# Kernel tuning notes

Hardware: AMD Instinct MI355X
Metric: run time of the kernel (lower is better)

Reference implementation:

```python
import jax, jax.numpy as jnp
import numpy as np

DEPTH = 4      # truncation depth of the signature
DIM = 8        # path channels
PATH_LEN = 16384
STREAM = True


def _restricted_exp(z, depth):
    # exp(z) in truncated tensor algebra: level k term = z^{\otimes k}/k!, flattened to [d**k]
    terms = [z]
    for k in range(2, depth + 1):
        terms.append((terms[-1][:, None] * z[None, :]).reshape(-1) / k)
    return tuple(terms)


def _chen_mult(a, b, depth):
    # Truncated tensor-algebra product (Chen's relation); a_0 = b_0 = 1 implicit.
    # c_k = a_k + b_k + sum_{i=1}^{k-1} a_i \otimes b_{k-i}
    c = []
    for k in range(depth):
        t = a[k] + b[k]
        for i in range(k):
            t = t + (a[i][:, None] * b[k - 1 - i][None, :]).reshape(-1)
        c.append(t)
    return tuple(c)


def setup_inputs() -> dict:
    key = jax.random.key(0)
    path = jax.random.normal(key, (PATH_LEN, DIM), dtype=jnp.float32)
    return {"path": path}


def reference(path):
    depth = DEPTH
    d = path.shape[-1]
    inc = path[1:] - path[:-1]                                # [N-1, d] increments
    exps = jax.vmap(lambda z: _restricted_exp(z, depth))(inc)  # tuple of [N-1, d**k]
    init = tuple(jnp.zeros((d ** (k + 1),), dtype=path.dtype) for k in range(depth))

    def step(carry, x):
        new = _chen_mult(carry, x, depth)
        return new, (new if STREAM else None)

    last, ys = jax.lax.scan(step, init, exps)
    if STREAM:
        # flatten: concat levels -> [N-1, d + d^2 + ... + d^depth]
        return jnp.concatenate([y for y in ys], axis=-1)
    return jnp.concatenate(last, axis=-1)
```

## Files before the change

### kernel.cpp

```cpp
#include <hip/hip_runtime.h>

#define NPATH 16384
#define DIM   8
#define NINC  (NPATH - 1)
#define SIG   4680
#define L1OFF 0
#define L2OFF 8
#define L3OFF 72
#define L4OFF 584
#define NCHUNK 256
#define CHUNK  64
#define NSUB  1024
#define SUB   16
#define SPC   4
#define NGRP  16
#define GSIZE 16
#define C6    0.16666666666666666f
#define LPAD  17

typedef float vfloat4 __attribute__((ext_vector_type(4)));
typedef float vfloat2 __attribute__((ext_vector_type(2)));


__device__ __forceinline__ void light_barrier() {
  asm volatile("s_waitcnt lgkmcnt(0)" ::: "memory");
  __builtin_amdgcn_s_barrier();
}

__device__ __forceinline__ void zero_state(float r4[16], float r3[2],
                                           float& a1i, float& a2v,
                                           float& a2s, float& a1s, float& a1t) {
#pragma unroll
  for (int l = 0; l < 16; ++l) r4[l] = 0.f;
  r3[0] = r3[1] = 0.f;
  a1i = a2v = a2s = a1s = a1t = 0.f;
}

__device__ __forceinline__ void store_sig_reg(float* __restrict__ dst,
                                              const float r4[16], const float r3[2],
                                              float a2s, float a1t, int t) {
  float4* d4 = (float4*)(dst + L4OFF + 16 * t);
  d4[0] = make_float4(r4[0], r4[1], r4[2], r4[3]);
  d4[1] = make_float4(r4[4], r4[5], r4[6], r4[7]);
  d4[2] = make_float4(r4[8], r4[9], r4[10], r4[11]);
  d4[3] = make_float4(r4[12], r4[13], r4[14], r4[15]);
  *(float2*)(dst + L3OFF + 2 * t) = make_float2(r3[0], r3[1]);
  if (t < 64) dst[L2OFF + t] = a2s;
  if (t < 8)  dst[L1OFF + t] = a1t;
}

struct ChenB {
  float4 B0, B1, B2, B3;
  float4 C0, C1, C2, C3;
  float4 D0, D1, D2, D3;
  float4 E0, E1;
  float2 b3c, b2jk, b1k;
  float  b2ij, b1j, b1i, b2t, b1j2, b1i2, b1t;
};

__device__ __forceinline__ void chen_load(const float* __restrict__ b, int t, ChenB& R) {
  const int i   = t >> 5;
  const int j   = (t >> 2) & 7;
  const int ij  = t >> 2;
  const int c0  = 2 * t;
  const int jk0 = c0 & 63;
  const int k0  = 2 * (t & 3);
  const int i2  = t >> 3;
  const int j2  = t & 7;
  const float4* bv = (const float4*)b;
  R.B0 = bv[146 + 4 * t]; R.B1 = bv[147 + 4 * t]; R.B2 = bv[148 + 4 * t]; R.B3 = bv[149 + 4 * t];
  R.C0 = bv[18 + 2 * jk0]; R.C1 = bv[19 + 2 * jk0]; R.C2 = bv[20 + 2 * jk0]; R.C3 = bv[21 + 2 * jk0];
  R.D0 = bv[2 + 2 * k0]; R.D1 = bv[3 + 2 * k0]; R.D2 = bv[4 + 2 * k0]; R.D3 = bv[5 + 2 * k0];
  R.E0 = bv[0]; R.E1 = bv[1];
  R.b3c  = *(const float2*)(b + L3OFF + c0);
  R.b2jk = *(const float2*)(b + L2OFF + jk0);
  R.b1k  = *(const float2*)(b + L1OFF + k0);
  R.b2ij = b[L2OFF + ij];
  R.b1j  = b[L1OFF + j];
  R.b1i  = b[L1OFF + i];
  R.b2t = 0.f; R.b1j2 = 0.f; R.b1i2 = 0.f; R.b1t = 0.f;
  if (t < 64) { R.b2t = b[L2OFF + t]; R.b1j2 = b[L1OFF + j2]; R.b1i2 = b[L1OFF + i2]; }
  if (t < 8)  { R.b1t = b[L1OFF + t]; }
}

__device__ __forceinline__ void chen_apply(float r4[16], float r3[2],
                                           float& a1i, float& a2v,
                                           float& a2s, float& a1s, float& a1t,
                                           const ChenB& R, int t) {
  const float b4r[16] = {R.B0.x,R.B0.y,R.B0.z,R.B0.w, R.B1.x,R.B1.y,R.B1.z,R.B1.w,
                         R.B2.x,R.B2.y,R.B2.z,R.B2.w, R.B3.x,R.B3.y,R.B3.z,R.B3.w};
  const float b3r[16] = {R.C0.x,R.C0.y,R.C0.z,R.C0.w, R.C1.x,R.C1.y,R.C1.z,R.C1.w,
                         R.C2.x,R.C2.y,R.C2.z,R.C2.w, R.C3.x,R.C3.y,R.C3.z,R.C3.w};
  const float b2r[16] = {R.D0.x,R.D0.y,R.D0.z,R.D0.w, R.D1.x,R.D1.y,R.D1.z,R.D1.w,
                         R.D2.x,R.D2.y,R.D2.z,R.D2.w, R.D3.x,R.D3.y,R.D3.z,R.D3.w};
  const float b1r[8]  = {R.E0.x,R.E0.y,R.E0.z,R.E0.w, R.E1.x,R.E1.y,R.E1.z,R.E1.w};
#pragma unroll
  for (int l = 0; l < 8; ++l) {
    r4[l]     += b4r[l]     + a1i * b3r[l]     + a2v * b2r[l]     + r3[0] * b1r[l];
    r4[8 + l] += b4r[8 + l] + a1i * b3r[8 + l] + a2v * b2r[8 + l] + r3[1] * b1r[l];
  }
  r3[0] += R.b3c.x + a1i * R.b2jk.x + a2v * R.b1k.x;
  r3[1] += R.b3c.y + a1i * R.b2jk.y + a2v * R.b1k.y;
  const float a1i_old = a1i;
  a2v += R.b2ij + a1i_old * R.b1j;
  if (t < 64) { a2s += R.b2t + a1s * R.b1j2; a1s += R.b1i2; }
  a1i = a1i_old + R.b1i;
  if (t < 8) a1t += R.b1t;
}

__device__ __forceinline__ void step_update(const float* zs,
                                            float r4[16], float r3[2],
                                            float& a1i, float& a2v,
                                            float& a2s, float& a1s, float& a1t, int t) {
  const int i  = t >> 5;
  const int j  = (t >> 2) & 7;
  const int k0 = 2 * (t & 3);
  const int i2 = t >> 3;
  const int j2 = t & 7;
  const float zi = zs[i];
  const float zj = zs[j];
  const float2 zk = *(const float2*)(zs + k0);
  const float4 za = *(const float4*)zs;
  const float4 zb = *(const float4*)(zs + 4);
  const float zn[8] = {za.x, za.y, za.z, za.w, zb.x, zb.y, zb.z, zb.w};
  const float a1zi4 = a1i + 0.25f * zi;
  const float zj6   = C6 * zj;
  const float T0 = r3[0] + a2v * (0.5f * zk.x) + a1zi4 * (zj6 * zk.x);
  const float T1 = r3[1] + a2v * (0.5f * zk.y) + a1zi4 * (zj6 * zk.y);
  const float U  = a2v + (0.5f * a1i + C6 * zi) * zj;
#pragma unroll
  for (int l = 0; l < 8; ++l) {
    r4[l]     += T0 * zn[l];
    r4[8 + l] += T1 * zn[l];
  }
  r3[0] += zk.x * U;
  r3[1] += zk.y * U;
  a2v += (a1i + 0.5f * zi) * zj;
  a1i += zi;
  if (t < 64) {
    const float zi2 = zs[i2], zj2v = zs[j2];
    a2s += (a1s + 0.5f * zi2) * zj2v;
    a1s += zi2;
  }
  if (t < 8) a1t += zs[t];
}

__global__ __launch_bounds__(256) void k_totals(const float* __restrict__ path,
                                                float* __restrict__ T64,
                                                float* __restrict__ snap) {
  __shared__ float zbuf[CHUNK][8];
  const int t = threadIdx.x;
  const int b = blockIdx.x;
  const int base = b * CHUNK;
  for (int u = t; u < CHUNK * 8; u += 256) {
    const int s = u >> 3, l = u & 7;
    const int rB = min(base + s + 1, NPATH - 1);
    zbuf[s][l] = path[rB * DIM + l] - path[(base + s) * DIM + l];
  }
  float r4[16], r3[2], a1i, a2v, a2s, a1s, a1t;
  zero_state(r4, r3, a1i, a2v, a2s, a1s, a1t);
  __syncthreads();
  for (int w = 0; w < SPC; ++w) {
    if (w > 0) store_sig_reg(snap + ((size_t)b * SPC + w) * SIG, r4, r3, a2s, a1t, t);
#pragma unroll
    for (int s2 = 0; s2 < SUB; ++s2)
      step_update(zbuf[SUB * w + s2], r4, r3, a1i, a2v, a2s, a1s, a1t, t);
  }
  store_sig_reg(T64 + (size_t)b * SIG, r4, r3, a2s, a1t, t);
}

__global__ __launch_bounds__(256) void k_scan(const float* __restrict__ in,
                                              float* __restrict__ prefout,
                                              float* __restrict__ totout,
                                              int count) {
  const int t = threadIdx.x;
  const size_t goff = (size_t)blockIdx.x * count;
  float r4[16], r3[2], a1i, a2v, a2s, a1s, a1t;
  zero_state(r4, r3, a1i, a2v, a2s, a1s, a1t);
  ChenB bA, bB;
  chen_load(in + goff * SIG, t, bA);
  for (int m = 0; m < count; m += 2) {
    if (m + 1 < count) chen_load(in + (goff + m + 1) * SIG, t, bB);
    store_sig_reg(prefout + (goff + m) * SIG, r4, r3, a2s, a1t, t);
    chen_apply(r4, r3, a1i, a2v, a2s, a1s, a1t, bA, t);
    if (m + 1 >= count) break;
    if (m + 2 < count) chen_load(in + (goff + m + 2) * SIG, t, bA);
    store_sig_reg(prefout + (goff + m + 1) * SIG, r4, r3, a2s, a1t, t);
    chen_apply(r4, r3, a1i, a2v, a2s, a1s, a1t, bB, t);
  }
  if (totout != nullptr) store_sig_reg(totout + (size_t)blockIdx.x * SIG, r4, r3, a2s, a1t, t);
}

__global__ __launch_bounds__(256) void k_out(const float* __restrict__ path,
                                             const float* __restrict__ pref,
                                             const float* __restrict__ GT,
                                             const float* __restrict__ snap,
                                             float* __restrict__ out) {
  __shared__ float zbuf[SUB][8];
  __shared__ __align__(16) float lbuf[2][256 * LPAD];
  const int t = threadIdx.x;
  const int sIdx = blockIdx.x;
  const int b = sIdx >> 2;
  const int g = b >> 4;
  const int base = sIdx * SUB;
  const int n = min(SUB, NINC - base);
  if (t < SUB * 8) {
    const int s = t >> 3, l = t & 7;
    const int rB = min(base + s + 1, NPATH - 1);
    zbuf[s][l] = path[rB * DIM + l] - path[(base + s) * DIM + l];
  }
  float r4[16], r3[2], a1i, a2v, a2s, a1s, a1t;
  zero_state(r4, r3, a1i, a2v, a2s, a1s, a1t);
  const int cnt = g + 1 + ((sIdx & 3) ? 1 : 0);
#define PADDR(m) ((m) < g ? GT + (size_t)(m) * SIG \
                          : ((m) == g ? pref + (size_t)b * SIG : snap + (size_t)sIdx * SIG))
  ChenB cA, cB;
  chen_load(PADDR(0), t, cA);
  for (int m = 0; m < cnt; m += 2) {
    if (m + 1 < cnt) chen_load(PADDR(m + 1), t, cB);
    chen_apply(r4, r3, a1i, a2v, a2s, a1s, a1t, cA, t);
    if (m + 1 >= cnt) break;
    if (m + 2 < cnt) chen_load(PADDR(m + 2), t, cA);
    chen_apply(r4, r3, a1i, a2v, a2s, a1s, a1t, cB, t);
  }
#undef PADDR
  __syncthreads();
  const int tp = t >> 2;
  const int rq = 4 * (t & 3);
#pragma unroll 4
  for (int s2 = 0; s2 < n; ++s2) {
    step_update(zbuf[s2], r4, r3, a1i, a2v, a2s, a1s, a1t, t);
    float* lb = lbuf[s2 & 1] + LPAD * t;
    *(float4*)(lb + 0)  = make_float4(r4[0], r4[1], r4[2], r4[3]);
    *(float4*)(lb + 4)  = make_float4(r4[4], r4[5], r4[6], r4[7]);
    *(float4*)(lb + 8)  = make_float4(r4[8], r4[9], r4[10], r4[11]);
    *(float4*)(lb + 12) = make_float4(r4[12], r4[13], r4[14], r4[15]);
    light_barrier();
    const float* lbr = lbuf[s2 & 1];
    float* dst = out + (size_t)(base + s2) * SIG;
#pragma unroll
    for (int q = 0; q < 4; ++q) {
      const vfloat4 v = *(const vfloat4*)(lbr + LPAD * (tp + 64 * q) + rq);
      __builtin_nontemporal_store(v, (vfloat4*)(dst + L4OFF + 4 * t + 1024 * q));
    }
    vfloat2 r3v; r3v.x = r3[0]; r3v.y = r3[1];
    __builtin_nontemporal_store(r3v, (vfloat2*)(dst + L3OFF + 2 * t));
    if (t < 64) __builtin_nontemporal_store(a2s, dst + L2OFF + t);
    if (t < 8)  __builtin_nontemporal_store(a1t, dst + L1OFF + t);
  }
}

extern "C" void kernel_launch(void* const* d_in, const int* in_sizes, int n_in,
                              void* d_out, int out_size, void* d_ws, size_t ws_size,
                              hipStream_t stream) {
  (void)in_sizes; (void)n_in; (void)out_size; (void)ws_size;
  const float* path = (const float*)d_in[0];
  float* out = (float*)d_out;
  float* ws = (float*)d_ws;

  float* T64    = ws;
  float* pref   = T64    + (size_t)NCHUNK * SIG;
  float* GT     = pref   + (size_t)NCHUNK * SIG;
  float* snap   = GT     + (size_t)NGRP * SIG;

  k_totals<<<NCHUNK, 256, 0, stream>>>(path, T64, snap);
  k_scan<<<NGRP, 256, 0, stream>>>(T64, pref, GT, GSIZE);
  k_out<<<NSUB, 256, 0, stream>>>(path, pref, GT, snap, out);
}
```

Before: 134.4 us.

## Remap k_out thread ownership so level-4 stores are direct without LDS transpose

Changes how level-3/4 signature elements are assigned to threads in the output kernel so each thread owns the contiguous float4 chunks it writes. The per-step LDS staging buffer and block barrier are removed, and a new Chen load/apply variant is written for the new mapping. Each thread now keeps redundant copies of lower-level state (four a1/a2/r3 values), which costs some extra registers and arithmetic per step.

```diff
diff --git a/kernel.cpp b/kernel.cpp
--- a/kernel.cpp
+++ b/kernel.cpp
@@ -16,16 +16,9 @@
 #define NGRP  16
 #define GSIZE 16
 #define C6    0.16666666666666666f
-#define LPAD  17
 
 typedef float vfloat4 __attribute__((ext_vector_type(4)));
-typedef float vfloat2 __attribute__((ext_vector_type(2)));
-
-
-__device__ __forceinline__ void light_barrier() {
-  asm volatile("s_waitcnt lgkmcnt(0)" ::: "memory");
-  __builtin_amdgcn_s_barrier();
-}
+
 
 __device__ __forceinline__ void zero_state(float r4[16], float r3[2],
                                            float& a1i, float& a2v,
@@ -191,13 +184,70 @@
   if (totout != nullptr) store_sig_reg(totout + (size_t)blockIdx.x * SIG, r4, r3, a2s, a1t, t);
 }
 
+
+struct ChenBN {
+  float4 B[4];
+  float4 C3r, D2r, E1r;
+  float  b3c[4];
+  float  b2jk, b1k, b1j;
+  float  b2ij[4];
+  float  b1i[4];
+  float  b2t, b1j2, b1i2, b1t;
+};
+
+__device__ __forceinline__ void chen_loadN(const float* __restrict__ b, int t, ChenBN& R) {
+  const int h  = t & 1;
+  const int th = t >> 1;
+  const int kk = th & 7;
+  const int jj = (th >> 3) & 7;
+  const int i0 = th >> 6;
+  const int jk = th & 63;
+#pragma unroll
+  for (int q = 0; q < 4; ++q) {
+    const int cq = th + 128 * q;
+    R.B[q]    = *(const float4*)(b + L4OFF + 8 * cq + 4 * h);
+    R.b3c[q]  = b[L3OFF + cq];
+    R.b2ij[q] = b[L2OFF + (i0 + 2 * q) * 8 + jj];
+    R.b1i[q]  = b[L1OFF + i0 + 2 * q];
+  }
+  R.C3r = *(const float4*)(b + L3OFF + 8 * jk + 4 * h);
+  R.D2r = *(const float4*)(b + L2OFF + 8 * kk + 4 * h);
+  R.E1r = *(const float4*)(b + L1OFF + 4 * h);
+  R.b2jk = b[L2OFF + jk];
+  R.b1k  = b[L1OFF + kk];
+  R.b1j  = b[L1OFF + jj];
+  R.b2t = 0.f; R.b1j2 = 0.f; R.b1i2 = 0.f; R.b1t = 0.f;
+  if (t < 64) { R.b2t = b[L2OFF + t]; R.b1j2 = b[L1OFF + (t & 7)]; R.b1i2 = b[L1OFF + (t >> 3)]; }
+  if (t < 8)  { R.b1t = b[L1OFF + t]; }
+}
+
+__device__ __forceinline__ void chen_applyN(float r4n[16], float r3n[4],
+                                            float a1n[4], float a2n[4],
+                                            float& a2s, float& a1s, float& a1t,
+                                            const ChenBN& R, int t) {
+  const float c3[4] = {R.C3r.x, R.C3r.y, R.C3r.z, R.C3r.w};
+  const float d2[4] = {R.D2r.x, R.D2r.y, R.D2r.z, R.D2r.w};
+  const float e1[4] = {R.E1r.x, R.E1r.y, R.E1r.z, R.E1r.w};
+#pragma unroll
+  for (int q = 0; q < 4; ++q) {
+    const float b4q[4] = {R.B[q].x, R.B[q].y, R.B[q].z, R.B[q].w};
+#pragma unroll
+    for (int u = 0; u < 4; ++u)
+      r4n[4 * q + u] += b4q[u] + a1n[q] * c3[u] + a2n[q] * d2[u] + r3n[q] * e1[u];
+    r3n[q] += R.b3c[q] + a1n[q] * R.b2jk + a2n[q] * R.b1k;
+    a2n[q] += R.b2ij[q] + a1n[q] * R.b1j;
+    a1n[q] += R.b1i[q];
+  }
+  if (t < 64) { a2s += R.b2t + a1s * R.b1j2; a1s += R.b1i2; }
+  if (t < 8)  a1t += R.b1t;
+}
+
 __global__ __launch_bounds__(256) void k_out(const float* __restrict__ path,
                                              const float* __restrict__ pref,
                                              const float* __restrict__ GT,
                                              const float* __restrict__ snap,
                                              float* __restrict__ out) {
   __shared__ float zbuf[SUB][8];
-  __shared__ __align__(16) float lbuf[2][256 * LPAD];
   const int t = threadIdx.x;
   const int sIdx = blockIdx.x;
   const int b = sIdx >> 2;
@@ -209,42 +259,67 @@
     const int rB = min(base + s + 1, NPATH - 1);
     zbuf[s][l] = path[rB * DIM + l] - path[(base + s) * DIM + l];
   }
-  float r4[16], r3[2], a1i, a2v, a2s, a1s, a1t;
-  zero_state(r4, r3, a1i, a2v, a2s, a1s, a1t);
+  const int h  = t & 1;
+  const int th = t >> 1;
+  const int kk = th & 7;
+  const int jj = (th >> 3) & 7;
+  const int i0 = th >> 6;
+  float r4n[16], r3n[4], a1n[4], a2n[4];
+#pragma unroll
+  for (int l = 0; l < 16; ++l) r4n[l] = 0.f;
+#pragma unroll
+  for (int q = 0; q < 4; ++q) { r3n[q] = 0.f; a1n[q] = 0.f; a2n[q] = 0.f; }
+  float a2s = 0.f, a1s = 0.f, a1t = 0.f;
   const int cnt = g + 1 + ((sIdx & 3) ? 1 : 0);
 #define PADDR(m) ((m) < g ? GT + (size_t)(m) * SIG \
                           : ((m) == g ? pref + (size_t)b * SIG : snap + (size_t)sIdx * SIG))
-  ChenB cA, cB;
-  chen_load(PADDR(0), t, cA);
+  ChenBN cA, cB;
+  chen_loadN(PADDR(0), t, cA);
   for (int m = 0; m < cnt; m += 2) {
-    if (m + 1 < cnt) chen_load(PADDR(m + 1), t, cB);
-    chen_apply(r4, r3, a1i, a2v, a2s, a1s, a1t, cA, t);
+    if (m + 1 < cnt) chen_loadN(PADDR(m + 1), t, cB);
+    chen_applyN(r4n, r3n, a1n, a2n, a2s, a1s, a1t, cA, t);
     if (m + 1 >= cnt) break;
-    if (m + 2 < cnt) chen_load(PADDR(m + 2), t, cA);
-    chen_apply(r4, r3, a1i, a2v, a2s, a1s, a1t, cB, t);
+    if (m + 2 < cnt) chen_loadN(PADDR(m + 2), t, cA);
+    chen_applyN(r4n, r3n, a1n, a2n, a2s, a1s, a1t, cB, t);
   }
 #undef PADDR
   __syncthreads();
-  const int tp = t >> 2;
-  const int rq = 4 * (t & 3);
+  const int qa = 2 * h;
 #pragma unroll 4
   for (int s2 = 0; s2 < n; ++s2) {
-    step_update(zbuf[s2], r4, r3, a1i, a2v, a2s, a1s, a1t, t);
-    float* lb = lbuf[s2 & 1] + LPAD * t;
-    *(float4*)(lb + 0)  = make_float4(r4[0], r4[1], r4[2], r4[3]);
-    *(float4*)(lb + 4)  = make_float4(r4[4], r4[5], r4[6], r4[7]);
-    *(float4*)(lb + 8)  = make_float4(r4[8], r4[9], r4[10], r4[11]);
-    *(float4*)(lb + 12) = make_float4(r4[12], r4[13], r4[14], r4[15]);
-    light_barrier();
-    const float* lbr = lbuf[s2 & 1];
+    const float* zs = zbuf[s2];
+    const float zk = zs[kk];
+    const float zj = zs[jj];
+    const float4 zlv = *(const float4*)(zs + 4 * h);
+    const float zl[4] = {zlv.x, zlv.y, zlv.z, zlv.w};
+    const float zi[4] = {zs[i0], zs[i0 + 2], zs[i0 + 4], zs[i0 + 6]};
+    const float halfzk = 0.5f * zk;
+    const float zj6zk  = (C6 * zj) * zk;
+#pragma unroll
+    for (int q = 0; q < 4; ++q) {
+      const float T = r3n[q] + a2n[q] * halfzk + (a1n[q] + 0.25f * zi[q]) * zj6zk;
+#pragma unroll
+      for (int u = 0; u < 4; ++u) r4n[4 * q + u] += T * zl[u];
+      const float U = a2n[q] + (0.5f * a1n[q] + C6 * zi[q]) * zj;
+      r3n[q] += zk * U;
+      a2n[q] += (a1n[q] + 0.5f * zi[q]) * zj;
+      a1n[q] += zi[q];
+    }
+    if (t < 64) {
+      const float zi2 = zs[t >> 3], zj2v = zs[t & 7];
+      a2s += (a1s + 0.5f * zi2) * zj2v;
+      a1s += zi2;
+    }
+    if (t < 8) a1t += zs[t];
     float* dst = out + (size_t)(base + s2) * SIG;
 #pragma unroll
     for (int q = 0; q < 4; ++q) {
-      const vfloat4 v = *(const vfloat4*)(lbr + LPAD * (tp + 64 * q) + rq);
+      vfloat4 v;
+      v.x = r4n[4 * q]; v.y = r4n[4 * q + 1]; v.z = r4n[4 * q + 2]; v.w = r4n[4 * q + 3];
       __builtin_nontemporal_store(v, (vfloat4*)(dst + L4OFF + 4 * t + 1024 * q));
     }
-    vfloat2 r3v; r3v.x = r3[0]; r3v.y = r3[1];
-    __builtin_nontemporal_store(r3v, (vfloat2*)(dst + L3OFF + 2 * t));
+    __builtin_nontemporal_store(r3n[qa],     dst + L3OFF + th + 128 * qa);
+    __builtin_nontemporal_store(r3n[qa + 1], dst + L3OFF + th + 128 * (qa + 1));
     if (t < 64) __builtin_nontemporal_store(a2s, dst + L2OFF + t);
     if (t < 8)  __builtin_nontemporal_store(a1t, dst + L1OFF + t);
   }
```

Measured after the change: 138.1 us. 1.03x slower.

## Restructure signature prefix scan into 16-step totals and 64-wide group scan

Applied to the files above, without the earlier changes.

Replaces the 64-step chunk totals kernel (256 blocks) with a 16-step kernel across 1024 blocks, then scans 64 sub-totals per group to produce per-subchunk snapshots directly. The output kernel then combines fewer prefix pieces: earlier group totals plus one snapshot, with no separate chunk prefix. This raises parallelism in the first stage, but the serial scan stage now does 64 Chen products per block instead of 16. Output stores also change from nontemporal builtins to plain vector stores.

```diff
diff --git a/kernel.cpp b/kernel.cpp
--- a/kernel.cpp
+++ b/kernel.cpp
@@ -8,18 +8,12 @@
 #define L2OFF 8
 #define L3OFF 72
 #define L4OFF 584
-#define NCHUNK 256
-#define CHUNK  64
 #define NSUB  1024
 #define SUB   16
-#define SPC   4
 #define NGRP  16
-#define GSIZE 16
+#define GSUB  64
 #define C6    0.16666666666666666f
 #define LPAD  17
-
-typedef float vfloat4 __attribute__((ext_vector_type(4)));
-typedef float vfloat2 __attribute__((ext_vector_type(2)));
 
 
 __device__ __forceinline__ void light_barrier() {
@@ -145,63 +139,56 @@
   if (t < 8) a1t += zs[t];
 }
 
-__global__ __launch_bounds__(256) void k_totals(const float* __restrict__ path,
-                                                float* __restrict__ T64,
-                                                float* __restrict__ snap) {
-  __shared__ float zbuf[CHUNK][8];
+__global__ __launch_bounds__(256) void k_t16(const float* __restrict__ path,
+                                             float* __restrict__ T16) {
+  __shared__ float zbuf[SUB][8];
   const int t = threadIdx.x;
-  const int b = blockIdx.x;
-  const int base = b * CHUNK;
-  for (int u = t; u < CHUNK * 8; u += 256) {
-    const int s = u >> 3, l = u & 7;
+  const int sIdx = blockIdx.x;
+  const int base = sIdx * SUB;
+  if (t < SUB * 8) {
+    const int s = t >> 3, l = t & 7;
     const int rB = min(base + s + 1, NPATH - 1);
     zbuf[s][l] = path[rB * DIM + l] - path[(base + s) * DIM + l];
   }
   float r4[16], r3[2], a1i, a2v, a2s, a1s, a1t;
   zero_state(r4, r3, a1i, a2v, a2s, a1s, a1t);
   __syncthreads();
-  for (int w = 0; w < SPC; ++w) {
-    if (w > 0) store_sig_reg(snap + ((size_t)b * SPC + w) * SIG, r4, r3, a2s, a1t, t);
-#pragma unroll
-    for (int s2 = 0; s2 < SUB; ++s2)
-      step_update(zbuf[SUB * w + s2], r4, r3, a1i, a2v, a2s, a1s, a1t, t);
-  }
-  store_sig_reg(T64 + (size_t)b * SIG, r4, r3, a2s, a1t, t);
-}
-
-__global__ __launch_bounds__(256) void k_scan(const float* __restrict__ in,
-                                              float* __restrict__ prefout,
-                                              float* __restrict__ totout,
-                                              int count) {
+#pragma unroll
+  for (int s2 = 0; s2 < SUB; ++s2)
+    step_update(zbuf[s2], r4, r3, a1i, a2v, a2s, a1s, a1t, t);
+  store_sig_reg(T16 + (size_t)sIdx * SIG, r4, r3, a2s, a1t, t);
+}
+
+__global__ __launch_bounds__(256) void k_scan2(const float* __restrict__ T16,
+                                               float* __restrict__ snapG,
+                                               float* __restrict__ GT) {
   const int t = threadIdx.x;
-  const size_t goff = (size_t)blockIdx.x * count;
+  const int g = blockIdx.x;
+  const size_t s0 = (size_t)g * GSUB;
   float r4[16], r3[2], a1i, a2v, a2s, a1s, a1t;
   zero_state(r4, r3, a1i, a2v, a2s, a1s, a1t);
   ChenB bA, bB;
-  chen_load(in + goff * SIG, t, bA);
-  for (int m = 0; m < count; m += 2) {
-    if (m + 1 < count) chen_load(in + (goff + m + 1) * SIG, t, bB);
-    store_sig_reg(prefout + (goff + m) * SIG, r4, r3, a2s, a1t, t);
+  chen_load(T16 + s0 * SIG, t, bA);
+  for (int m = 0; m < GSUB; m += 2) {
+    chen_load(T16 + (s0 + m + 1) * SIG, t, bB);
+    if (m) store_sig_reg(snapG + (s0 + m) * SIG, r4, r3, a2s, a1t, t);
     chen_apply(r4, r3, a1i, a2v, a2s, a1s, a1t, bA, t);
-    if (m + 1 >= count) break;
-    if (m + 2 < count) chen_load(in + (goff + m + 2) * SIG, t, bA);
-    store_sig_reg(prefout + (goff + m + 1) * SIG, r4, r3, a2s, a1t, t);
+    if (m + 2 < GSUB) chen_load(T16 + (s0 + m + 2) * SIG, t, bA);
+    store_sig_reg(snapG + (s0 + m + 1) * SIG, r4, r3, a2s, a1t, t);
     chen_apply(r4, r3, a1i, a2v, a2s, a1s, a1t, bB, t);
   }
-  if (totout != nullptr) store_sig_reg(totout + (size_t)blockIdx.x * SIG, r4, r3, a2s, a1t, t);
+  store_sig_reg(GT + (size_t)g * SIG, r4, r3, a2s, a1t, t);
 }
 
 __global__ __launch_bounds__(256) void k_out(const float* __restrict__ path,
-                                             const float* __restrict__ pref,
+                                             const float* __restrict__ snapG,
                                              const float* __restrict__ GT,
-                                             const float* __restrict__ snap,
                                              float* __restrict__ out) {
   __shared__ float zbuf[SUB][8];
   __shared__ __align__(16) float lbuf[2][256 * LPAD];
   const int t = threadIdx.x;
   const int sIdx = blockIdx.x;
-  const int b = sIdx >> 2;
-  const int g = b >> 4;
+  const int g = sIdx >> 6;
   const int base = sIdx * SUB;
   const int n = min(SUB, NINC - base);
   if (t < SUB * 8) {
@@ -211,17 +198,18 @@
   }
   float r4[16], r3[2], a1i, a2v, a2s, a1s, a1t;
   zero_state(r4, r3, a1i, a2v, a2s, a1s, a1t);
-  const int cnt = g + 1 + ((sIdx & 3) ? 1 : 0);
-#define PADDR(m) ((m) < g ? GT + (size_t)(m) * SIG \
-                          : ((m) == g ? pref + (size_t)b * SIG : snap + (size_t)sIdx * SIG))
-  ChenB cA, cB;
-  chen_load(PADDR(0), t, cA);
-  for (int m = 0; m < cnt; m += 2) {
-    if (m + 1 < cnt) chen_load(PADDR(m + 1), t, cB);
-    chen_apply(r4, r3, a1i, a2v, a2s, a1s, a1t, cA, t);
-    if (m + 1 >= cnt) break;
-    if (m + 2 < cnt) chen_load(PADDR(m + 2), t, cA);
-    chen_apply(r4, r3, a1i, a2v, a2s, a1s, a1t, cB, t);
+  const int cnt = g + ((sIdx & 63) ? 1 : 0);
+#define PADDR(m) ((m) < g ? GT + (size_t)(m) * SIG : snapG + (size_t)sIdx * SIG)
+  if (cnt > 0) {
+    ChenB cA, cB;
+    chen_load(PADDR(0), t, cA);
+    for (int m = 0; m < cnt; m += 2) {
+      if (m + 1 < cnt) chen_load(PADDR(m + 1), t, cB);
+      chen_apply(r4, r3, a1i, a2v, a2s, a1s, a1t, cA, t);
+      if (m + 1 >= cnt) break;
+      if (m + 2 < cnt) chen_load(PADDR(m + 2), t, cA);
+      chen_apply(r4, r3, a1i, a2v, a2s, a1s, a1t, cB, t);
+    }
   }
 #undef PADDR
   __syncthreads();
@@ -240,13 +228,12 @@
     float* dst = out + (size_t)(base + s2) * SIG;
 #pragma unroll
     for (int q = 0; q < 4; ++q) {
-      const vfloat4 v = *(const vfloat4*)(lbr + LPAD * (tp + 64 * q) + rq);
-      __builtin_nontemporal_store(v, (vfloat4*)(dst + L4OFF + 4 * t + 1024 * q));
+      const float4 v = *(const float4*)(lbr + LPAD * (tp + 64 * q) + rq);
+      *(float4*)(dst + L4OFF + 4 * t + 1024 * q) = v;
     }
-    vfloat2 r3v; r3v.x = r3[0]; r3v.y = r3[1];
-    __builtin_nontemporal_store(r3v, (vfloat2*)(dst + L3OFF + 2 * t));
-    if (t < 64) __builtin_nontemporal_store(a2s, dst + L2OFF + t);
-    if (t < 8)  __builtin_nontemporal_store(a1t, dst + L1OFF + t);
+    *(float2*)(dst + L3OFF + 2 * t) = make_float2(r3[0], r3[1]);
+    if (t < 64) dst[L2OFF + t] = a2s;
+    if (t < 8)  dst[L1OFF + t] = a1t;
   }
 }
 
@@ -258,12 +245,11 @@
   float* out = (float*)d_out;
   float* ws = (float*)d_ws;
 
-  float* T64    = ws;
-  float* pref   = T64    + (size_t)NCHUNK * SIG;
-  float* GT     = pref   + (size_t)NCHUNK * SIG;
-  float* snap   = GT     + (size_t)NGRP * SIG;
-
-  k_totals<<<NCHUNK, 256, 0, stream>>>(path, T64, snap);
-  k_scan<<<NGRP, 256, 0, stream>>>(T64, pref, GT, GSIZE);
-  k_out<<<NSUB, 256, 0, stream>>>(path, pref, GT, snap, out);
-}
+  float* GT    = ws;
+  float* snapG = GT    + (size_t)NGRP * SIG;
+  float* T16   = snapG + (size_t)NSUB * SIG;
+
+  k_t16<<<NSUB, 256, 0, stream>>>(path, T16);
+  k_scan2<<<NGRP, 256, 0, stream>>>(T16, snapG, GT);
+  k_out<<<NSUB, 256, 0, stream>>>(path, snapG, GT, out);
+}
```

Result: slower. 197.1 us (+46.7%).
